# Kernel tuning notes

Measured on AMD Instinct MI355X. Metric: run time of the kernel, lower is better.

The kernel has to match this reference:

```python
import jax, jax.numpy as jnp
import numpy as np

B, S, D, H = 2, 2048, 1024, 16
DK = D // H  # 64, per-head key/value dim


def setup_inputs() -> dict:
    key = jax.random.key(0)
    ks = jax.random.split(key, 8)
    q = jax.random.normal(ks[0], (B, S, D), dtype=jnp.float32)
    k = jax.random.normal(ks[1], (B, S, D), dtype=jnp.float32)
    v = jax.random.normal(ks[2], (B, S, D), dtype=jnp.float32)
    # per-head projection weights, initialized like torch.randn in the original
    W_q = jax.random.normal(ks[3], (H, D, DK), dtype=jnp.float32)
    W_k = jax.random.normal(ks[4], (H, D, DK), dtype=jnp.float32)
    W_v = jax.random.normal(ks[5], (H, D, DK), dtype=jnp.float32)
    # output nn.Linear(H*DK, D): weight [D, H*DK], bias [D]
    bound = 1.0 / np.sqrt(H * DK)
    W_o = jax.random.uniform(ks[6], (D, H * DK), dtype=jnp.float32, minval=-bound, maxval=bound)
    b_o = jax.random.uniform(ks[7], (D,), dtype=jnp.float32, minval=-bound, maxval=bound)
    return {"q": q, "k": k, "v": v, "W_q": W_q, "W_k": W_k, "W_v": W_v, "W_o": W_o, "b_o": b_o}


def reference(q, k, v, W_q, W_k, W_v, W_o, b_o):
    dk = W_q.shape[-1]
    # batched per-head projections (replaces the Python loop over heads)
    qh = jnp.einsum('bsd,hdk->bhsk', q, W_q)  # [B,H,S,DK]
    kh = jnp.einsum('bsd,hdk->bhsk', k, W_k)
    vh = jnp.einsum('bsd,hdk->bhsk', v, W_v)
    scale = jnp.asarray(np.sqrt(dk), qh.dtype)
    scores = jnp.einsum('bhsk,bhtk->bhst', qh, kh) / scale  # [B,H,S,S]
    attn = jax.nn.softmax(scores, axis=-1)
    ctx = jnp.einsum('bhst,bhtk->bhsk', attn, vh)  # [B,H,S,DK]
    # concat heads along feature dim (matches torch.cat(..., dim=2))
    b, h, s, d = ctx.shape
    ctx = ctx.transpose(0, 2, 1, 3).reshape(b, s, h * d)  # [B,S,H*DK]
    return ctx @ W_o.T + b_o  # [B,S,D]
```

## Files before the change

kernel.cpp:

```cpp
#include <hip/hip_runtime.h>
#include <math.h>

#define B_ 2
#define S_ 2048
#define D_ 1024
#define H_ 16
#define ATTN_C 0.18033688011f

typedef unsigned short ushort_t;
typedef __attribute__((ext_vector_type(8))) short short8;
typedef __attribute__((ext_vector_type(4))) short short4v;
typedef __attribute__((ext_vector_type(4))) float f32x4;
typedef __attribute__((ext_vector_type(2))) float f32x2;
typedef __attribute__((ext_vector_type(16))) float f32x16;
typedef __attribute__((ext_vector_type(4))) unsigned int uint4v;

#define MFMA(A, B, C) __builtin_amdgcn_mfma_f32_32x32x16_bf16((A), (B), (C), 0, 0, 0)
#define Z16 {0.f,0.f,0.f,0.f,0.f,0.f,0.f,0.f,0.f,0.f,0.f,0.f,0.f,0.f,0.f,0.f}

__device__ __forceinline__ ushort_t bf16rn(float x) {
    unsigned int u = __builtin_bit_cast(unsigned int, x);
    u += 0x7FFFu + ((u >> 16) & 1u);
    return (ushort_t)(u >> 16);
}
__device__ __forceinline__ float bf16tof(ushort_t h) {
    return __builtin_bit_cast(float, (unsigned int)h << 16);
}
__device__ __forceinline__ unsigned cvtpk(float lo, float hi) {
    unsigned r;
    asm("v_cvt_pk_bf16_f32 %0, %1, %2" : "=v"(r) : "v"(lo), "v"(hi));
    return r;
}
__device__ __forceinline__ void gload16(const void* g, void* l) {
    __builtin_amdgcn_global_load_lds(
        (const __attribute__((address_space(1))) unsigned int*)(unsigned long long)g,
        (__attribute__((address_space(3))) unsigned int*)(unsigned int)(unsigned long long)l,
        16, 0, 0);
}

__global__ __launch_bounds__(256) void cvtx_kernel(
    const float* __restrict__ Xq, const float* __restrict__ Xk,
    const float* __restrict__ Xv,
    ushort_t* __restrict__ Xh, ushort_t* __restrict__ Xl)
{
    const int pr = blockIdx.y;
    const float* X = pr == 0 ? Xq : pr == 1 ? Xk : Xv;
    const size_t idx = ((size_t)blockIdx.x * 256 + threadIdx.x) * 8;
    f32x4 v0 = *(const f32x4*)(X + idx);
    f32x4 v1 = *(const f32x4*)(X + idx + 4);
    float f[8] = {v0.x, v0.y, v0.z, v0.w, v1.x, v1.y, v1.z, v1.w};
    short8 hi, lo;
#pragma unroll
    for (int i = 0; i < 8; ++i) {
        ushort_t hh = bf16rn(f[i]);
        hi[i] = (short)hh;
        lo[i] = (short)bf16rn(f[i] - bf16tof(hh));
    }
    const size_t base = (size_t)pr * 2 * S_ * D_;
    *(short8*)(Xh + base + idx) = hi;
    if (pr < 2) *(short8*)(Xl + base + idx) = lo;
}

__global__ __launch_bounds__(256) void cvtw_kernel(
    const float* __restrict__ Wq, const float* __restrict__ Wk,
    const float* __restrict__ Wv,
    ushort_t* __restrict__ wqh, ushort_t* __restrict__ wql,
    ushort_t* __restrict__ wkh, ushort_t* __restrict__ wkl,
    ushort_t* __restrict__ wvh)
{
    __shared__ float T[64][68];
    const int dt = blockIdx.x, h = blockIdx.y, mat = blockIdx.z;
    const int tid = threadIdx.x;
    const float* W = mat == 0 ? Wq : mat == 1 ? Wk : Wv;
    const float* Wb = W + ((size_t)h * 1024 + dt * 64) * 64;
#pragma unroll
    for (int u = 0; u < 4; ++u) {
        int idx = tid + u * 256;
        int d = idx >> 4, c4 = idx & 15;
        f32x4 v = *(const f32x4*)(Wb + (size_t)d * 64 + c4 * 4);
        T[d][c4 * 4 + 0] = v.x; T[d][c4 * 4 + 1] = v.y;
        T[d][c4 * 4 + 2] = v.z; T[d][c4 * 4 + 3] = v.w;
    }
    __syncthreads();
    ushort_t* oh = mat == 0 ? wqh : mat == 1 ? wkh : wvh;
    ushort_t* ol = mat == 0 ? wql : mat == 1 ? wkl : nullptr;
#pragma unroll
    for (int u = 0; u < 4; ++u) {
        int idx = tid + u * 256;
        int n = idx >> 4, c4 = idx & 15;
        float v0 = T[c4 * 4 + 0][n], v1 = T[c4 * 4 + 1][n];
        float v2 = T[c4 * 4 + 2][n], v3 = T[c4 * 4 + 3][n];
        ushort_t h0 = bf16rn(v0), h1 = bf16rn(v1), h2 = bf16rn(v2), h3 = bf16rn(v3);
        size_t off = ((size_t)h * 64 + n) * 1024 + dt * 64 + c4 * 4;
        short4v hv = {(short)h0, (short)h1, (short)h2, (short)h3};
        *(short4v*)(oh + off) = hv;
        if (ol) {
            short4v lv = {(short)bf16rn(v0 - bf16tof(h0)), (short)bf16rn(v1 - bf16tof(h1)),
                          (short)bf16rn(v2 - bf16tof(h2)), (short)bf16rn(v3 - bf16tof(h3))};
            *(short4v*)(ol + off) = lv;
        }
    }
}

__global__ __launch_bounds__(256) void cvtwo_kernel(
    const float* __restrict__ Wo, ushort_t* __restrict__ wob)
{
    size_t idx = (size_t)blockIdx.x * 256 + threadIdx.x;
    f32x4 v = *(const f32x4*)(Wo + idx * 4);
    short4v o = {(short)bf16rn(v.x), (short)bf16rn(v.y),
                 (short)bf16rn(v.z), (short)bf16rn(v.w)};
    *(short4v*)(wob + idx * 4) = o;
}

__global__ __launch_bounds__(256, 2) void proj_kernel(
    const ushort_t* __restrict__ Xh, const ushort_t* __restrict__ Xl,
    const ushort_t* __restrict__ Wh_q, const ushort_t* __restrict__ Wl_q,
    const ushort_t* __restrict__ Wh_k, const ushort_t* __restrict__ Wl_k,
    const ushort_t* __restrict__ Wh_v,
    ushort_t* __restrict__ Oq_h, ushort_t* __restrict__ Oq_l,
    ushort_t* __restrict__ Ok_h, ushort_t* __restrict__ Ok_l,
    ushort_t* __restrict__ Ovt)
{
    __shared__ __align__(16) ushort_t Xs[128 * 128];
    __shared__ __align__(16) ushort_t Ws[128 * 128];
    const int tid = threadIdx.x;
    const int wv = tid >> 6, lane = tid & 63;
    const int lo32 = lane & 31, g = lane >> 5;
    const int wm = wv >> 1, wn = wv & 1;
    const int lrow = lane >> 4, lg = lane & 15;
    const int m0 = blockIdx.x * 128;
    const int n0 = blockIdx.y * 128;
    const int pr = blockIdx.z >> 1, b = blockIdx.z & 1;
    const bool split = (pr != 2);
    const ushort_t* Whp = pr == 0 ? Wh_q : pr == 1 ? Wh_k : Wh_v;
    const ushort_t* Wlp = pr == 0 ? Wl_q : pr == 1 ? Wl_k : Wh_v;
    const ushort_t* Xhb = Xh + ((size_t)(pr * 2 + b) * S_ + m0) * D_;
    const ushort_t* Xlb = Xl + ((size_t)(pr * 2 + b) * S_ + m0) * D_;
    f32x16 a00 = Z16, a01 = Z16, a10 = Z16, a11 = Z16;

    for (int d0 = 0; d0 < D_; d0 += 64) {
        __syncthreads();
#pragma unroll
        for (int u = 0; u < 8; ++u) {
            int row = u * 16 + wv * 4 + lrow;
            int gs = lg ^ (row & 15);
            int half = gs >> 3, c8 = gs & 7;
            const ushort_t* srcX = ((half && split) ? Xlb : Xhb) + (size_t)row * D_ + d0 + c8 * 8;
            gload16(srcX, (char*)Xs + (u * 16 + wv * 4) * 256);
            const ushort_t* srcW = ((half && split) ? Wlp : Whp) + (size_t)(n0 + row) * 1024 + d0 + c8 * 8;
            gload16(srcW, (char*)Ws + (u * 16 + wv * 4) * 256);
        }
        __syncthreads();
#pragma unroll
        for (int ks = 0; ks < 4; ++ks) {
            int coff = ks * 16 + g * 8;
            int r0 = wm * 64 + lo32, r1 = r0 + 32;
            int c0 = wn * 64 + lo32, c1 = c0 + 32;
            short8 a0h = *(const short8*)&Xs[(r0 * 128 + coff) ^ ((r0 & 15) << 3)];
            short8 a1h = *(const short8*)&Xs[(r1 * 128 + coff) ^ ((r1 & 15) << 3)];
            short8 b0h = *(const short8*)&Ws[(c0 * 128 + coff) ^ ((c0 & 15) << 3)];
            short8 b1h = *(const short8*)&Ws[(c1 * 128 + coff) ^ ((c1 & 15) << 3)];
            a00 = MFMA(a0h, b0h, a00);
            a01 = MFMA(a0h, b1h, a01);
            a10 = MFMA(a1h, b0h, a10);
            a11 = MFMA(a1h, b1h, a11);
            if (split) {
                short8 a0l = *(const short8*)&Xs[(r0 * 128 + 64 + coff) ^ ((r0 & 15) << 3)];
                short8 a1l = *(const short8*)&Xs[(r1 * 128 + 64 + coff) ^ ((r1 & 15) << 3)];
                short8 b0l = *(const short8*)&Ws[(c0 * 128 + 64 + coff) ^ ((c0 & 15) << 3)];
                short8 b1l = *(const short8*)&Ws[(c1 * 128 + 64 + coff) ^ ((c1 & 15) << 3)];
                a00 = MFMA(a0h, b0l, a00); a00 = MFMA(a0l, b0h, a00);
                a01 = MFMA(a0h, b1l, a01); a01 = MFMA(a0l, b1h, a01);
                a10 = MFMA(a1h, b0l, a10); a10 = MFMA(a1l, b0h, a10);
                a11 = MFMA(a1h, b1l, a11); a11 = MFMA(a1l, b1h, a11);
            }
        }
    }
    ushort_t* OH = pr == 0 ? Oq_h : pr == 1 ? Ok_h : Ovt;
    ushort_t* OL = pr == 0 ? Oq_l : pr == 1 ? Ok_l : Ovt;
    const bool qscale = (pr == 0);
#define PROJ_STORE(ACC, MT, NT)                                               \
    _Pragma("unroll")                                                         \
    for (int r = 0; r < 16; ++r) {                                            \
        int s_loc = m0 + wm * 64 + (MT) * 32 + (r & 3) + 8 * (r >> 2) + 4 * g;\
        int col = n0 + wn * 64 + (NT) * 32 + lo32;                            \
        int hh_ = col >> 6, nn = col & 63;                                    \
        float val = ACC[r];                                                   \
        if (qscale) val *= ATTN_C;                                            \
        if (split) {                                                          \
            size_t off = (((size_t)b * H_ + hh_) * S_ + s_loc) * 64 + nn;     \
            ushort_t hv = bf16rn(val);                                        \
            OH[off] = hv;                                                     \
            OL[off] = bf16rn(val - bf16tof(hv));                              \
        } else {                                                              \
            size_t offt = (((size_t)b * H_ + hh_) * 64 + nn) * S_ + s_loc;    \
            OH[offt] = bf16rn(val);                                           \
        }                                                                     \
    }
    PROJ_STORE(a00, 0, 0)
    PROJ_STORE(a01, 0, 1)
    PROJ_STORE(a10, 1, 0)
    PROJ_STORE(a11, 1, 1)
#undef PROJ_STORE
}

__global__ __launch_bounds__(256, 2) void attn_kernel(
    const ushort_t* __restrict__ qh_h, const ushort_t* __restrict__ qh_l,
    const ushort_t* __restrict__ kh_h, const ushort_t* __restrict__ kh_l,
    const ushort_t* __restrict__ vt, ushort_t* __restrict__ Opart,
    float* __restrict__ Ml)
{
    __shared__ __align__(16) char smem[32768];
    ushort_t* Vt = (ushort_t*)smem;
    const int tid = threadIdx.x;
    const int wv = tid >> 6, lane = tid & 63;
    const int lo32 = lane & 31, g = lane >> 5;
    const int s0 = blockIdx.x * 256;
    const int h = blockIdx.y;
    const int b = blockIdx.z >> 1, sp = blockIdx.z & 1;
    const size_t bhs = ((size_t)b * H_ + h) * S_ * 64;

    short8 qfh[2][4], qfl[2][4];
#pragma unroll
    for (int c = 0; c < 2; ++c) {
        const ushort_t* Qrh = qh_h + bhs + (size_t)(s0 + wv * 64 + c * 32 + lo32) * 64;
        const ushort_t* Qrl = qh_l + bhs + (size_t)(s0 + wv * 64 + c * 32 + lo32) * 64;
#pragma unroll
        for (int ks = 0; ks < 4; ++ks) {
            qfh[c][ks] = *(const short8*)(Qrh + ks * 16 + g * 8);
            qfl[c][ks] = *(const short8*)(Qrl + ks * 16 + g * 8);
        }
    }
    const ushort_t* Kgh = kh_h + bhs;
    const ushort_t* Kgl = kh_l + bhs;
    const ushort_t* Vtg = vt + ((size_t)b * H_ + h) * 64 * S_;

    f32x16 o00 = Z16, o01 = Z16, o10 = Z16, o11 = Z16;
    float mrun0 = -3.0e38f, mrun1 = -3.0e38f;
    float lrun0 = 0.f, lrun1 = 0.f;
    const int kvbeg = sp * (S_ / 2);

#define MAX16(ST) fmaxf(fmaxf(fmaxf(fmaxf(ST[0], ST[1]), fmaxf(ST[2], ST[3])),   \
                              fmaxf(fmaxf(ST[4], ST[5]), fmaxf(ST[6], ST[7]))),  \
                        fmaxf(fmaxf(fmaxf(ST[8], ST[9]), fmaxf(ST[10], ST[11])), \
                              fmaxf(fmaxf(ST[12], ST[13]), fmaxf(ST[14], ST[15]))))

#define SOFTMAX_PV(ST, CME, MR, LR, OA, OB)                                   \
    {                                                                         \
        if (__any(CME > MR)) {                                                \
            float mnew = fmaxf(MR, CME);                                      \
            float corr = __builtin_amdgcn_exp2f(MR - mnew);                   \
            LR *= corr;                                                       \
            _Pragma("unroll")                                                 \
            for (int r = 0; r < 16; ++r) { OA[r] *= corr; OB[r] *= corr; }    \
            MR = mnew;                                                        \
        }                                                                     \
        float p[16], ls = 0.f;                                                \
        _Pragma("unroll")                                                     \
        for (int r = 0; r < 16; ++r) {                                        \
            p[r] = __builtin_amdgcn_exp2f(ST[r] - MR);                        \
            ls += p[r];                                                       \
        }                                                                     \
        LR += ls;                                                             \
        {                                                                     \
            unsigned w0 = cvtpk(p[0], p[1]), w1 = cvtpk(p[2], p[3]);          \
            unsigned w2 = cvtpk(p[4], p[5]), w3 = cvtpk(p[6], p[7]);          \
            asm("v_permlane32_swap_b32 %0, %1" : "+v"(w0), "+v"(w2));         \
            asm("v_permlane32_swap_b32 %0, %1" : "+v"(w1), "+v"(w3));         \
            uint4v pa = {w0, w1, w2, w3};                                     \
            short8 pf = __builtin_bit_cast(short8, pa);                       \
            OA = MFMA(vfa0, pf, OA);                                          \
            OB = MFMA(vfa1, pf, OB);                                          \
            w0 = cvtpk(p[8], p[9]);  w1 = cvtpk(p[10], p[11]);                \
            w2 = cvtpk(p[12], p[13]); w3 = cvtpk(p[14], p[15]);               \
            asm("v_permlane32_swap_b32 %0, %1" : "+v"(w0), "+v"(w2));         \
            asm("v_permlane32_swap_b32 %0, %1" : "+v"(w1), "+v"(w3));         \
            uint4v pb = {w0, w1, w2, w3};                                     \
            short8 pf2 = __builtin_bit_cast(short8, pb);                      \
            OA = MFMA(vfb0, pf2, OA);                                         \
            OB = MFMA(vfb1, pf2, OB);                                         \
        }                                                                     \
    }

#define LOADK(CI, DH, DL)                                                     \
    {                                                                         \
        int cc = (CI) > 31 ? 31 : (CI);                                       \
        const ushort_t* pn = Kgh + (size_t)(kvbeg + cc * 32 + lo32) * 64 + g * 8; \
        DH[0] = *(const short8*)(pn);                                         \
        DH[1] = *(const short8*)(pn + 16);                                    \
        DH[2] = *(const short8*)(pn + 32);                                    \
        DH[3] = *(const short8*)(pn + 48);                                    \
        const ushort_t* pl = Kgl + (size_t)(kvbeg + cc * 32 + lo32) * 64 + g * 8; \
        DL[0] = *(const short8*)(pl);                                         \
        DL[1] = *(const short8*)(pl + 16);                                    \
        DL[2] = *(const short8*)(pl + 32);                                    \
        DL[3] = *(const short8*)(pl + 48);                                    \
    }

#define CHUNK_BODY(KH, KL, KHN, KLN, CI)                                      \
    {                                                                         \
        LOADK((CI) + 1, KHN, KLN);                                            \
        f32x16 st0 = Z16, st1 = Z16;                                          \
        st0 = MFMA(KH[0], qfh[0][0], st0); st1 = MFMA(KH[0], qfh[1][0], st1); \
        st0 = MFMA(KH[1], qfh[0][1], st0); st1 = MFMA(KH[1], qfh[1][1], st1); \
        st0 = MFMA(KH[2], qfh[0][2], st0); st1 = MFMA(KH[2], qfh[1][2], st1); \
        st0 = MFMA(KH[3], qfh[0][3], st0); st1 = MFMA(KH[3], qfh[1][3], st1); \
        st0 = MFMA(KL[0], qfh[0][0], st0); st1 = MFMA(KL[0], qfh[1][0], st1); \
        st0 = MFMA(KL[1], qfh[0][1], st0); st1 = MFMA(KL[1], qfh[1][1], st1); \
        st0 = MFMA(KL[2], qfh[0][2], st0); st1 = MFMA(KL[2], qfh[1][2], st1); \
        st0 = MFMA(KL[3], qfh[0][3], st0); st1 = MFMA(KL[3], qfh[1][3], st1); \
        st0 = MFMA(KH[0], qfl[0][0], st0); st1 = MFMA(KH[0], qfl[1][0], st1); \
        st0 = MFMA(KH[1], qfl[0][1], st0); st1 = MFMA(KH[1], qfl[1][1], st1); \
        st0 = MFMA(KH[2], qfl[0][2], st0); st1 = MFMA(KH[2], qfl[1][2], st1); \
        st0 = MFMA(KH[3], qfl[0][3], st0); st1 = MFMA(KH[3], qfl[1][3], st1); \
        const int kvb = ((CI) & 7) * 32;                                      \
        const int vsw = (lo32 & 15) << 3;                                     \
        float cm0 = MAX16(st0);                                               \
        float cm1 = MAX16(st1);                                               \
        cm0 = fmaxf(cm0, __shfl_xor(cm0, 32));                                \
        cm1 = fmaxf(cm1, __shfl_xor(cm1, 32));                                \
        short8 vfa0 = *(const short8*)&Vt[(lo32 * 256 + kvb + g * 8) ^ vsw];        \
        short8 vfa1 = *(const short8*)&Vt[((lo32 + 32) * 256 + kvb + g * 8) ^ vsw]; \
        short8 vfb0 = *(const short8*)&Vt[(lo32 * 256 + kvb + 16 + g * 8) ^ vsw];   \
        short8 vfb1 = *(const short8*)&Vt[((lo32 + 32) * 256 + kvb + 16 + g * 8) ^ vsw]; \
        if (__any(cm0 > mrun0 - 126.f)) SOFTMAX_PV(st0, cm0, mrun0, lrun0, o00, o01) \
        if (__any(cm1 > mrun1 - 126.f)) SOFTMAX_PV(st1, cm1, mrun1, lrun1, o10, o11) \
    }

    short8 ka_h[4], ka_l[4], kb_h[4], kb_l[4];
    LOADK(0, ka_h, ka_l);
    int c = 0;
    for (int t = 0; t < 4; ++t) {
        const int kv0 = kvbeg + t * 256;
        __syncthreads();
#pragma unroll
        for (int u = 0; u < 8; ++u) {
            int rowb = u * 8 + wv * 2;
            int d = rowb + (lane >> 5);
            const ushort_t* src = Vtg + (size_t)d * S_ + kv0 + 8 * ((lane & 31) ^ (d & 15));
            gload16(src, (char*)Vt + rowb * 512);
        }
        __syncthreads();
        CHUNK_BODY(ka_h, ka_l, kb_h, kb_l, c + 0)
        CHUNK_BODY(kb_h, kb_l, ka_h, ka_l, c + 1)
        CHUNK_BODY(ka_h, ka_l, kb_h, kb_l, c + 2)
        CHUNK_BODY(kb_h, kb_l, ka_h, ka_l, c + 3)
        CHUNK_BODY(ka_h, ka_l, kb_h, kb_l, c + 4)
        CHUNK_BODY(kb_h, kb_l, ka_h, ka_l, c + 5)
        CHUNK_BODY(ka_h, ka_l, kb_h, kb_l, c + 6)
        CHUNK_BODY(kb_h, kb_l, ka_h, ka_l, c + 7)
        c += 8;
    }
#undef CHUNK_BODY
#undef LOADK
#undef SOFTMAX_PV
#undef MAX16

    lrun0 += __shfl_xor(lrun0, 32);
    lrun1 += __shfl_xor(lrun1, 32);
    __syncthreads();
    float* Oe = ((float*)smem) + wv * 2048;
    const size_t orowb = (size_t)sp * (B_ * H_ * S_) + ((size_t)b * H_ + h) * S_ + s0 + wv * 64;
#pragma unroll
    for (int r = 0; r < 16; ++r) {
        int dd = (r & 3) + 8 * (r >> 2) + 4 * g;
        int qsw = (lo32 & 7) << 2;
        Oe[(lo32 * 64 + dd) ^ qsw] = o00[r];
        Oe[(lo32 * 64 + 32 + dd) ^ qsw] = o01[r];
    }
#pragma unroll
    for (int rep = 0; rep < 8; ++rep) {
        int idx = lane + rep * 64;
        int qq = idx >> 4, d4 = idx & 15;
        f32x4 ov = *(const f32x4*)&Oe[(qq * 64 + d4 * 4) ^ ((qq & 7) << 2)];
        short4v pk4 = {(short)bf16rn(ov.x), (short)bf16rn(ov.y),
                       (short)bf16rn(ov.z), (short)bf16rn(ov.w)};
        *(short4v*)(Opart + (orowb + qq) * 64 + d4 * 4) = pk4;
    }
    if (g == 0) {
        f32x2 ml = {mrun0, lrun0};
        *(f32x2*)(Ml + (orowb + lo32) * 2) = ml;
    }
    __builtin_amdgcn_s_waitcnt(0);
#pragma unroll
    for (int r = 0; r < 16; ++r) {
        int dd = (r & 3) + 8 * (r >> 2) + 4 * g;
        int qsw = (lo32 & 7) << 2;
        Oe[(lo32 * 64 + dd) ^ qsw] = o10[r];
        Oe[(lo32 * 64 + 32 + dd) ^ qsw] = o11[r];
    }
#pragma unroll
    for (int rep = 0; rep < 8; ++rep) {
        int idx = lane + rep * 64;
        int qq = idx >> 4, d4 = idx & 15;
        f32x4 ov = *(const f32x4*)&Oe[(qq * 64 + d4 * 4) ^ ((qq & 7) << 2)];
        short4v pk4 = {(short)bf16rn(ov.x), (short)bf16rn(ov.y),
                       (short)bf16rn(ov.z), (short)bf16rn(ov.w)};
        *(short4v*)(Opart + (orowb + 32 + qq) * 64 + d4 * 4) = pk4;
    }
    if (g == 0) {
        f32x2 ml = {mrun1, lrun1};
        *(f32x2*)(Ml + (orowb + 32 + lo32) * 2) = ml;
    }
}

__global__ __launch_bounds__(256) void merge_kernel(
    const ushort_t* __restrict__ Opart, const float* __restrict__ Ml,
    ushort_t* __restrict__ ctxb)
{
    const int NROW = B_ * H_ * S_;
    int gidx = blockIdx.x * 256 + threadIdx.x;
    int row = gidx >> 3, d8 = (gidx & 7) * 8;
    f32x2 ml0 = *(const f32x2*)(Ml + (size_t)row * 2);
    f32x2 ml1 = *(const f32x2*)(Ml + ((size_t)NROW + row) * 2);
    float M = fmaxf(ml0.x, ml1.x);
    float w0 = __builtin_amdgcn_exp2f(ml0.x - M);
    float w1 = __builtin_amdgcn_exp2f(ml1.x - M);
    float inv = 1.f / (ml0.y * w0 + ml1.y * w1);
    w0 *= inv; w1 *= inv;
    short8 a = *(const short8*)(Opart + (size_t)row * 64 + d8);
    short8 c = *(const short8*)(Opart + ((size_t)NROW + row) * 64 + d8);
    short8 o;
#pragma unroll
    for (int i = 0; i < 8; ++i) {
        float f = bf16tof((ushort_t)a[i]) * w0 + bf16tof((ushort_t)c[i]) * w1;
        o[i] = (short)bf16rn(f);
    }
    int bb = row >> 15, hh = (row >> 11) & 15, s = row & 2047;
    *(short8*)(ctxb + ((size_t)bb * S_ + s) * D_ + hh * 64 + d8) = o;
}

__global__ __launch_bounds__(128, 2) void outproj_kernel(
    const ushort_t* __restrict__ ctxb, const ushort_t* __restrict__ wob,
    const float* __restrict__ bo, float* __restrict__ Out)
{
    __shared__ __align__(16) ushort_t Cs[128 * 128];
    __shared__ __align__(16) ushort_t Ws2[64 * 128];
    const int tid = threadIdx.x;
    const int wv = tid >> 6, lane = tid & 63;
    const int lo32 = lane & 31, g = lane >> 5;
    const int lrow = lane >> 4, lg = lane & 15;
    const int n0 = blockIdx.x * 64;
    const int m0 = blockIdx.y * 128;
    f32x16 a00 = Z16, a01 = Z16, a10 = Z16, a11 = Z16;
    for (int k0 = 0; k0 < D_; k0 += 128) {
        __syncthreads();
#pragma unroll
        for (int u = 0; u < 16; ++u) {
            int row = u * 8 + wv * 4 + lrow;
            int gs = lg ^ (row & 15);
            const ushort_t* src = ctxb + (size_t)(m0 + row) * D_ + k0 + gs * 8;
            gload16(src, (char*)Cs + (u * 8 + wv * 4) * 256);
        }
#pragma unroll
        for (int u = 0; u < 8; ++u) {
            int row = u * 8 + wv * 4 + lrow;
            int gs = lg ^ (row & 15);
            const ushort_t* src = wob + (size_t)(n0 + row) * D_ + k0 + gs * 8;
            gload16(src, (char*)Ws2 + (u * 8 + wv * 4) * 256);
        }
        __syncthreads();
#pragma unroll
        for (int ks = 0; ks < 8; ++ks) {
            int coff = ks * 16 + g * 8;
            int r0 = wv * 64 + lo32, r1 = r0 + 32;
            int n1 = lo32 + 32;
            short8 A0 = *(const short8*)&Cs[(r0 * 128 + coff) ^ ((r0 & 15) << 3)];
            short8 A1 = *(const short8*)&Cs[(r1 * 128 + coff) ^ ((r1 & 15) << 3)];
            short8 B0 = *(const short8*)&Ws2[(lo32 * 128 + coff) ^ ((lo32 & 15) << 3)];
            short8 B1 = *(const short8*)&Ws2[(n1 * 128 + coff) ^ ((n1 & 15) << 3)];
            a00 = MFMA(A0, B0, a00);
            a01 = MFMA(A0, B1, a01);
            a10 = MFMA(A1, B0, a10);
            a11 = MFMA(A1, B1, a11);
        }
    }
    float b0v = bo[n0 + lo32], b1v = bo[n0 + 32 + lo32];
#define OUT_STORE(ACC, MT, NT, BV)                                          \
    _Pragma("unroll")                                                       \
    for (int r = 0; r < 16; ++r) {                                          \
        int m = m0 + wv * 64 + (MT) * 32 + (r & 3) + 8 * (r >> 2) + 4 * g;  \
        int n = n0 + (NT) * 32 + lo32;                                      \
        Out[(size_t)m * D_ + n] = ACC[r] + (BV);                            \
    }
    OUT_STORE(a00, 0, 0, b0v)
    OUT_STORE(a01, 0, 1, b1v)
    OUT_STORE(a10, 1, 0, b0v)
    OUT_STORE(a11, 1, 1, b1v)
#undef OUT_STORE
}

extern "C" void kernel_launch(void* const* d_in, const int* in_sizes, int n_in,
                              void* d_out, int out_size, void* d_ws,
                              size_t ws_size, hipStream_t stream)
{
    const float* q = (const float*)d_in[0];
    const float* k = (const float*)d_in[1];
    const float* v = (const float*)d_in[2];
    const float* W_q = (const float*)d_in[3];
    const float* W_k = (const float*)d_in[4];
    const float* W_v = (const float*)d_in[5];
    const float* W_o = (const float*)d_in[6];
    const float* b_o = (const float*)d_in[7];
    float* out = (float*)d_out;

    ushort_t* wqt_h = (ushort_t*)d_ws;
    ushort_t* wqt_l = wqt_h + (1 << 20);
    ushort_t* wkt_h = wqt_l + (1 << 20);
    ushort_t* wkt_l = wkt_h + (1 << 20);
    ushort_t* wvt_h = wkt_l + (1 << 20);
    ushort_t* wob   = wvt_h + (1 << 20);
    ushort_t* qh_h  = wob + (1 << 20);
    ushort_t* qh_l  = qh_h + (1 << 22);
    ushort_t* kh_h  = qh_l + (1 << 22);
    ushort_t* kh_l  = kh_h + (1 << 22);
    ushort_t* vtp   = kh_l + (1 << 22);
    ushort_t* Xh    = vtp + (1 << 22);
    ushort_t* Xl    = Xh + 3 * (1 << 22);
    ushort_t* ctxb  = Xh;
    ushort_t* Opart = Xl;
    float*    Ml    = (float*)(Xl + 2 * (size_t)(B_ * H_ * S_) * 64);

    cvtx_kernel<<<dim3(2048, 3), 256, 0, stream>>>(q, k, v, Xh, Xl);
    cvtw_kernel<<<dim3(16, 16, 3), 256, 0, stream>>>(
        W_q, W_k, W_v, wqt_h, wqt_l, wkt_h, wkt_l, wvt_h);
    cvtwo_kernel<<<1024, 256, 0, stream>>>(W_o, wob);
    proj_kernel<<<dim3(16, 8, 6), 256, 0, stream>>>(
        Xh, Xl, wqt_h, wqt_l, wkt_h, wkt_l, wvt_h,
        qh_h, qh_l, kh_h, kh_l, vtp);
    attn_kernel<<<dim3(8, 16, 4), 256, 0, stream>>>(
        qh_h, qh_l, kh_h, kh_l, vtp, Opart, Ml);
    merge_kernel<<<2048, 256, 0, stream>>>(Opart, Ml, ctxb);
    outproj_kernel<<<dim3(16, 32), 128, 0, stream>>>(ctxb, wob, b_o, out);
}
```

Measured before the change: 269.1 us.

## Skip low-order QK correction MFMAs for chunks the softmax will ignore

Score computation first uses only the high bf16 parts of Q and K. The lo-part correction MFMAs, the V fragment loads and softmax/PV run only when a chunk's coarse max comes within 64 of the running max, with a refined 30 threshold afterwards. This removes two thirds of the QK MFMAs on chunks whose scores underflow to zero. The K low parts are now loaded without prefetch, so they may stall, and the extra branches and approximate thresholds could lose accuracy.

```diff
diff --git a/kernel.cpp b/kernel.cpp
--- a/kernel.cpp
+++ b/kernel.cpp
@@ -282,7 +282,7 @@
         }                                                                     \
     }
 
-#define LOADK(CI, DH, DL)                                                     \
+#define LOADKHI(CI, DH)                                                       \
     {                                                                         \
         int cc = (CI) > 31 ? 31 : (CI);                                       \
         const ushort_t* pn = Kgh + (size_t)(kvbeg + cc * 32 + lo32) * 64 + g * 8; \
@@ -290,45 +290,63 @@
         DH[1] = *(const short8*)(pn + 16);                                    \
         DH[2] = *(const short8*)(pn + 32);                                    \
         DH[3] = *(const short8*)(pn + 48);                                    \
-        const ushort_t* pl = Kgl + (size_t)(kvbeg + cc * 32 + lo32) * 64 + g * 8; \
-        DL[0] = *(const short8*)(pl);                                         \
-        DL[1] = *(const short8*)(pl + 16);                                    \
-        DL[2] = *(const short8*)(pl + 32);                                    \
-        DL[3] = *(const short8*)(pl + 48);                                    \
-    }
-
-#define CHUNK_BODY(KH, KL, KHN, KLN, CI)                                      \
+    }
+
+#define CHUNK_BODY(KH, KHN, CI)                                               \
     {                                                                         \
-        LOADK((CI) + 1, KHN, KLN);                                            \
+        LOADKHI((CI) + 1, KHN);                                               \
+        const ushort_t* pl = Kgl + (size_t)(kvbeg + (CI) * 32 + lo32) * 64 + g * 8; \
+        short8 kl0 = *(const short8*)(pl);                                    \
+        short8 kl1 = *(const short8*)(pl + 16);                               \
+        short8 kl2 = *(const short8*)(pl + 32);                               \
+        short8 kl3 = *(const short8*)(pl + 48);                               \
         f32x16 st0 = Z16, st1 = Z16;                                          \
         st0 = MFMA(KH[0], qfh[0][0], st0); st1 = MFMA(KH[0], qfh[1][0], st1); \
         st0 = MFMA(KH[1], qfh[0][1], st0); st1 = MFMA(KH[1], qfh[1][1], st1); \
         st0 = MFMA(KH[2], qfh[0][2], st0); st1 = MFMA(KH[2], qfh[1][2], st1); \
         st0 = MFMA(KH[3], qfh[0][3], st0); st1 = MFMA(KH[3], qfh[1][3], st1); \
-        st0 = MFMA(KL[0], qfh[0][0], st0); st1 = MFMA(KL[0], qfh[1][0], st1); \
-        st0 = MFMA(KL[1], qfh[0][1], st0); st1 = MFMA(KL[1], qfh[1][1], st1); \
-        st0 = MFMA(KL[2], qfh[0][2], st0); st1 = MFMA(KL[2], qfh[1][2], st1); \
-        st0 = MFMA(KL[3], qfh[0][3], st0); st1 = MFMA(KL[3], qfh[1][3], st1); \
-        st0 = MFMA(KH[0], qfl[0][0], st0); st1 = MFMA(KH[0], qfl[1][0], st1); \
-        st0 = MFMA(KH[1], qfl[0][1], st0); st1 = MFMA(KH[1], qfl[1][1], st1); \
-        st0 = MFMA(KH[2], qfl[0][2], st0); st1 = MFMA(KH[2], qfl[1][2], st1); \
-        st0 = MFMA(KH[3], qfl[0][3], st0); st1 = MFMA(KH[3], qfl[1][3], st1); \
-        const int kvb = ((CI) & 7) * 32;                                      \
-        const int vsw = (lo32 & 15) << 3;                                     \
         float cm0 = MAX16(st0);                                               \
         float cm1 = MAX16(st1);                                               \
         cm0 = fmaxf(cm0, __shfl_xor(cm0, 32));                                \
         cm1 = fmaxf(cm1, __shfl_xor(cm1, 32));                                \
-        short8 vfa0 = *(const short8*)&Vt[(lo32 * 256 + kvb + g * 8) ^ vsw];        \
-        short8 vfa1 = *(const short8*)&Vt[((lo32 + 32) * 256 + kvb + g * 8) ^ vsw]; \
-        short8 vfb0 = *(const short8*)&Vt[(lo32 * 256 + kvb + 16 + g * 8) ^ vsw];   \
-        short8 vfb1 = *(const short8*)&Vt[((lo32 + 32) * 256 + kvb + 16 + g * 8) ^ vsw]; \
-        if (__any(cm0 > mrun0 - 126.f)) SOFTMAX_PV(st0, cm0, mrun0, lrun0, o00, o01) \
-        if (__any(cm1 > mrun1 - 126.f)) SOFTMAX_PV(st1, cm1, mrun1, lrun1, o10, o11) \
-    }
-
-    short8 ka_h[4], ka_l[4], kb_h[4], kb_l[4];
-    LOADK(0, ka_h, ka_l);
+        const bool need0 = __any(cm0 > mrun0 - 64.f);                         \
+        const bool need1 = __any(cm1 > mrun1 - 64.f);                         \
+        if (need0 | need1) {                                                  \
+            if (need0) {                                                      \
+                st0 = MFMA(KH[0], qfl[0][0], st0); st0 = MFMA(kl0, qfh[0][0], st0); \
+                st0 = MFMA(KH[1], qfl[0][1], st0); st0 = MFMA(kl1, qfh[0][1], st0); \
+                st0 = MFMA(KH[2], qfl[0][2], st0); st0 = MFMA(kl2, qfh[0][2], st0); \
+                st0 = MFMA(KH[3], qfl[0][3], st0); st0 = MFMA(kl3, qfh[0][3], st0); \
+            }                                                                 \
+            if (need1) {                                                      \
+                st1 = MFMA(KH[0], qfl[1][0], st1); st1 = MFMA(kl0, qfh[1][0], st1); \
+                st1 = MFMA(KH[1], qfl[1][1], st1); st1 = MFMA(kl1, qfh[1][1], st1); \
+                st1 = MFMA(KH[2], qfl[1][2], st1); st1 = MFMA(kl2, qfh[1][2], st1); \
+                st1 = MFMA(KH[3], qfl[1][3], st1); st1 = MFMA(kl3, qfh[1][3], st1); \
+            }                                                                 \
+            const int kvb = ((CI) & 7) * 32;                                  \
+            const int vsw = (lo32 & 15) << 3;                                 \
+            short8 vfa0 = *(const short8*)&Vt[(lo32 * 256 + kvb + g * 8) ^ vsw];        \
+            short8 vfa1 = *(const short8*)&Vt[((lo32 + 32) * 256 + kvb + g * 8) ^ vsw]; \
+            short8 vfb0 = *(const short8*)&Vt[(lo32 * 256 + kvb + 16 + g * 8) ^ vsw];   \
+            short8 vfb1 = *(const short8*)&Vt[((lo32 + 32) * 256 + kvb + 16 + g * 8) ^ vsw]; \
+            if (need0) {                                                      \
+                float cme = MAX16(st0);                                       \
+                cme = fmaxf(cme, __shfl_xor(cme, 32));                        \
+                if (__any(cme > mrun0 - 30.f))                                \
+                    SOFTMAX_PV(st0, cme, mrun0, lrun0, o00, o01)              \
+            }                                                                 \
+            if (need1) {                                                      \
+                float cme = MAX16(st1);                                       \
+                cme = fmaxf(cme, __shfl_xor(cme, 32));                        \
+                if (__any(cme > mrun1 - 30.f))                                \
+                    SOFTMAX_PV(st1, cme, mrun1, lrun1, o10, o11)              \
+            }                                                                 \
+        }                                                                     \
+    }
+
+    short8 ka_h[4], kb_h[4];
+    LOADKHI(0, ka_h);
     int c = 0;
     for (int t = 0; t < 4; ++t) {
         const int kv0 = kvbeg + t * 256;
@@ -341,18 +359,18 @@
             gload16(src, (char*)Vt + rowb * 512);
         }
         __syncthreads();
-        CHUNK_BODY(ka_h, ka_l, kb_h, kb_l, c + 0)
-        CHUNK_BODY(kb_h, kb_l, ka_h, ka_l, c + 1)
-        CHUNK_BODY(ka_h, ka_l, kb_h, kb_l, c + 2)
-        CHUNK_BODY(kb_h, kb_l, ka_h, ka_l, c + 3)
-        CHUNK_BODY(ka_h, ka_l, kb_h, kb_l, c + 4)
-        CHUNK_BODY(kb_h, kb_l, ka_h, ka_l, c + 5)
-        CHUNK_BODY(ka_h, ka_l, kb_h, kb_l, c + 6)
-        CHUNK_BODY(kb_h, kb_l, ka_h, ka_l, c + 7)
+        CHUNK_BODY(ka_h, kb_h, c + 0)
+        CHUNK_BODY(kb_h, ka_h, c + 1)
+        CHUNK_BODY(ka_h, kb_h, c + 2)
+        CHUNK_BODY(kb_h, ka_h, c + 3)
+        CHUNK_BODY(ka_h, kb_h, c + 4)
+        CHUNK_BODY(kb_h, ka_h, c + 5)
+        CHUNK_BODY(ka_h, kb_h, c + 6)
+        CHUNK_BODY(kb_h, ka_h, c + 7)
         c += 8;
     }
 #undef CHUNK_BODY
-#undef LOADK
+#undef LOADKHI
 #undef SOFTMAX_PV
 #undef MAX16
 
```

After: 284.3 us. 5.6% more time.
